# Kernel tuning notes

Measured on AMD Instinct MI355X. Metric: run time of the kernel, lower is better.

## Reference

```python
import jax, jax.numpy as jnp
import numpy as np

DIM, D_STATE, D_CONV, EXPAND = 384, 16, 4, 2
D_INNER = EXPAND * DIM          # 768
DT_RANK = -(-DIM // 16)         # 24
B_, T_, H_, W_ = 2, 8, 16, 16
EPS = 1e-5


def layernorm(x, w, b):
    mu = x.mean(-1, keepdims=True)
    var = ((x - mu) ** 2).mean(-1, keepdims=True)
    return (x - mu) * jax.lax.rsqrt(var + EPS) * w + b


def setup_inputs() -> dict:
    key = jax.random.key(0)
    ks = jax.random.split(key, 12)
    std = 0.02
    x = jax.random.normal(ks[0], (B_, DIM, T_, H_, W_), jnp.float32)
    params = dict(
        ln1_w=jnp.ones((DIM,), jnp.float32),
        ln1_b=jnp.zeros((DIM,), jnp.float32),
        ln2_w=jnp.ones((DIM,), jnp.float32),
        ln2_b=jnp.zeros((DIM,), jnp.float32),
        in_proj_w=std * jax.random.normal(ks[1], (2 * D_INNER, DIM), jnp.float32),
        conv_w=std * jax.random.normal(ks[2], (D_INNER, 1, D_CONV), jnp.float32),
        conv_b=jnp.zeros((D_INNER,), jnp.float32),
        x_proj_w=std * jax.random.normal(ks[3], (DT_RANK + 2 * D_STATE, D_INNER), jnp.float32),
        dt_proj_w=std * jax.random.normal(ks[4], (D_INNER, DT_RANK), jnp.float32),
        dt_proj_b=0.01 * jax.random.normal(ks[5], (D_INNER,), jnp.float32),
        A_log=jnp.log(jnp.broadcast_to(jnp.arange(1, D_STATE + 1, dtype=jnp.float32), (D_INNER, D_STATE))),
        D=jnp.ones((D_INNER,), jnp.float32),
        out_proj_w=std * jax.random.normal(ks[6], (DIM, D_INNER), jnp.float32),
    )
    return {"x": x, **params}


def mamba(xn, in_proj_w, conv_w, conv_b, x_proj_w, dt_proj_w, dt_proj_b, A_log, D, out_proj_w):
    # xn: [B, L, dim]
    B, L, _ = xn.shape
    xz = xn @ in_proj_w.T                      # [B, L, 2*d_inner]
    u, z = jnp.split(xz, 2, axis=-1)
    # causal depthwise conv over tokens
    uc = jnp.transpose(u, (0, 2, 1))           # [B, d_inner, L]
    uc = jax.lax.conv_general_dilated(
        uc, conv_w, window_strides=(1,), padding=[(D_CONV - 1, 0)],
        dimension_numbers=("NCH", "OIH", "NCH"), feature_group_count=D_INNER)
    u = jax.nn.silu(jnp.transpose(uc, (0, 2, 1)) + conv_b)  # [B, L, d_inner]

    dbc = u @ x_proj_w.T                       # [B, L, dt_rank + 2*d_state]
    dt = dbc[..., :DT_RANK]
    Bm = dbc[..., DT_RANK:DT_RANK + D_STATE]   # [B, L, d_state]
    Cm = dbc[..., DT_RANK + D_STATE:]          # [B, L, d_state]
    delta = jax.nn.softplus(dt @ dt_proj_w.T + dt_proj_b)   # [B, L, d_inner]

    A = -jnp.exp(A_log)                        # [d_inner, d_state]
    deltaA = jnp.exp(delta[..., None] * A)                     # [B, L, d_inner, d_state]
    deltaBu = delta[..., None] * Bm[:, :, None, :] * u[..., None]

    def step(h, inp):
        dA, dBu, c = inp                       # [B,d_inner,d_state], [B,d_inner,d_state], [B,d_state]
        h = dA * h + dBu
        y = jnp.einsum("bds,bs->bd", h, c)
        return h, y

    h0 = jnp.zeros((B, D_INNER, D_STATE), xn.dtype)
    xs = (jnp.moveaxis(deltaA, 1, 0), jnp.moveaxis(deltaBu, 1, 0), jnp.moveaxis(Cm, 1, 0))
    _, ys = jax.lax.scan(step, h0, xs)
    y = jnp.moveaxis(ys, 0, 1)                 # [B, L, d_inner]
    y = y + u * D
    y = y * jax.nn.silu(z)
    return y @ out_proj_w.T                    # [B, L, dim]


def reference(x, ln1_w, ln1_b, ln2_w, ln2_b, in_proj_w, conv_w, conv_b,
              x_proj_w, dt_proj_w, dt_proj_b, A_log, D, out_proj_w):
    B, C, T, H, W = x.shape
    L = T * H * W
    x_flat = jnp.transpose(x.reshape(B, C, L), (0, 2, 1))   # [B, L, C]
    x_norm = layernorm(x_flat, ln1_w, ln1_b)
    x_mamba = mamba(x_norm, in_proj_w, conv_w, conv_b, x_proj_w,
                    dt_proj_w, dt_proj_b, A_log, D, out_proj_w)
    x_out = layernorm(x_flat + x_mamba, ln2_w, ln2_b)
    return jnp.transpose(x_out, (0, 2, 1)).reshape(B, C, T, H, W)
```

## Files before the change

kernel.cpp:

```cpp
#include <hip/hip_runtime.h>
#include <hip/hip_bf16.h>

typedef unsigned short u16;
typedef unsigned int   u32;
typedef __attribute__((ext_vector_type(8))) short short8;
typedef __attribute__((ext_vector_type(4))) float f32x4;

#define B_   2
#define L_   2048
#define CDIM 384
#define DI   768
#define DXZ  1536
#define DTR  24
#define DS   16
#define NDBC 56
#define NC2  128
#define TC   16
#define TL   32
#define EPSV 1e-5f

#define OFFW_WIN  0
#define OFFW_WXP  589824
#define OFFW_WOUT 632832
#define TOTW      927744

__device__ __forceinline__ float bf2f(u16 u) {
    union { u32 i; float f; } v; v.i = ((u32)u) << 16; return v.f;
}
__device__ __forceinline__ u16 f2bf(float f) {
    union { float f; u32 i; } v; v.f = f;
    u32 x = v.i;
    u32 r = (x + 0x7FFFu + ((x >> 16) & 1u)) >> 16;
    return (u16)r;
}

__global__ __launch_bounds__(256) void ln1_convert(const float* __restrict__ x,
                                                   const float* __restrict__ w,
                                                   const float* __restrict__ bb,
                                                   u16* __restrict__ xn,
                                                   const float* __restrict__ win,
                                                   const float* __restrict__ wxp,
                                                   const float* __restrict__ wout,
                                                   u16* __restrict__ wdst) {
    __shared__ float tile[CDIM][TL + 1];
    __shared__ float red_s[8][TL];
    __shared__ float red_s2[8][TL];
    __shared__ float mu_s[TL], rs_s[TL];
    int tid = threadIdx.x, blk = blockIdx.x;
    if (blk >= 128) {
        int base = (blk - 128) * 256 + tid;
        for (int e = base; e < TOTW; e += 128 * 256) {
            float v;
            if (e < OFFW_WXP)       v = win[e];
            else if (e < OFFW_WOUT) v = wxp[e - OFFW_WXP];
            else                    v = wout[e - OFFW_WOUT];
            wdst[e] = f2bf(v);
        }
        return;
    }
    int b = blk >> 6;
    int l0 = (blk & 63) * TL;
    int cg = tid >> 5, li = tid & 31;
    const float* xp = x + (size_t)b * CDIM * L_ + l0 + li;
    float s = 0.f, s2 = 0.f;
#pragma unroll
    for (int c = cg; c < CDIM; c += 8) {
        float v = xp[(size_t)c * L_];
        tile[c][li] = v;
        s += v; s2 += v * v;
    }
    red_s[cg][li] = s; red_s2[cg][li] = s2;
    __syncthreads();
    if (tid < TL) {
        float ts = 0.f, ts2 = 0.f;
#pragma unroll
        for (int g = 0; g < 8; g++) { ts += red_s[g][tid]; ts2 += red_s2[g][tid]; }
        float mu = ts / CDIM;
        float var = ts2 / CDIM - mu * mu;
        mu_s[tid] = mu; rs_s[tid] = rsqrtf(var + EPSV);
    }
    __syncthreads();
    int wv = tid >> 6, lane = tid & 63;
#pragma unroll
    for (int r = 0; r < 8; r++) {
        int l = wv * 8 + r;
        float mu = mu_s[l], rs = rs_s[l];
        u16* op = xn + (size_t)(b * L_ + l0 + l) * CDIM;
#pragma unroll
        for (int j = 0; j < 6; j++) {
            int c = lane + 64 * j;
            float t = (tile[c][l] - mu) * rs * w[c] + bb[c];
            op[c] = f2bf(t);
        }
    }
}

template<int KN>
__global__ __launch_bounds__(256) void gemm_in(const u16* __restrict__ A,
                                               const u16* __restrict__ Bm,
                                               u16* __restrict__ Cp, int Nn) {
    int wave = threadIdx.x >> 6, lane = threadIdx.x & 63;
    int wm = wave & 1, wn = wave >> 1;
    int m0 = (blockIdx.x * 2 + wm) * 64;
    int n0 = (blockIdx.y * 2 + wn) * 64;
    int r = lane & 15, q = lane >> 4;
    f32x4 acc[4][4];
#pragma unroll
    for (int i = 0; i < 4; i++)
#pragma unroll
        for (int j = 0; j < 4; j++)
#pragma unroll
            for (int g = 0; g < 4; g++) acc[i][j][g] = 0.f;
#pragma unroll
    for (int k0 = 0; k0 < KN; k0 += 32) {
        short8 af[4], bf[4];
        int ka = k0 + q * 8;
#pragma unroll
        for (int i = 0; i < 4; i++) {
            af[i] = *(const short8*)(A + (size_t)(m0 + i * 16 + r) * KN + ka);
            bf[i] = *(const short8*)(Bm + (size_t)(n0 + i * 16 + r) * KN + ka);
        }
#pragma unroll
        for (int i = 0; i < 4; i++)
#pragma unroll
            for (int j = 0; j < 4; j++)
                acc[i][j] = __builtin_amdgcn_mfma_f32_16x16x32_bf16(af[i], bf[j], acc[i][j], 0, 0, 0);
    }
#pragma unroll
    for (int i = 0; i < 4; i++)
#pragma unroll
        for (int j = 0; j < 4; j++) {
            int col = n0 + j * 16 + r;
#pragma unroll
            for (int g = 0; g < 4; g++)
                Cp[(size_t)(m0 + i * 16 + q * 4 + g) * Nn + col] = f2bf(acc[i][j][g]);
        }
}

__global__ __launch_bounds__(768) void convxp_scan1(const u16* __restrict__ xz,
                                                    const float* __restrict__ cw,
                                                    const float* __restrict__ cb,
                                                    const u16* __restrict__ wxpb,
                                                    const float* __restrict__ alogf,
                                                    const float* __restrict__ wdtf,
                                                    const float* __restrict__ bdtf,
                                                    float* __restrict__ dbc,
                                                    float* __restrict__ chA,
                                                    float* __restrict__ chB) {
    __shared__ __align__(16) u16 uS[TC * DI];
    __shared__ float smR[6][TC][60];
    __shared__ float dbcS[TC][60];
    int tid = threadIdx.x;
    int bc = blockIdx.x;
    int b = bc >> 7, chunk = bc & 127;
    int t0g = b * L_ + chunk * TC;
    float ur[TC];
    {
        int d = tid;
        float4 c4 = ((const float4*)cw)[d];
        float bias = cb[d];
        float w0, w1, w2;
        if (chunk == 0) { w0 = w1 = w2 = 0.f; }
        else {
            w0 = bf2f(xz[(size_t)(t0g - 3) * DXZ + d]);
            w1 = bf2f(xz[(size_t)(t0g - 2) * DXZ + d]);
            w2 = bf2f(xz[(size_t)(t0g - 1) * DXZ + d]);
        }
#pragma unroll
        for (int t = 0; t < TC; t++) {
            float cur = bf2f(xz[(size_t)(t0g + t) * DXZ + d]);
            float acc = bias + w0 * c4.x + w1 * c4.y + w2 * c4.z + cur * c4.w;
            float sg = 1.f / (1.f + __expf(-acc));
            ur[t] = acc * sg;
            uS[t * DI + (d ^ ((t & 7) << 3))] = f2bf(ur[t]);
            w0 = w1; w1 = w2; w2 = cur;
        }
    }
    __syncthreads();
    {
        int wave = tid >> 6, lane = tid & 63;
        int r = lane & 15, q = lane >> 4;
        if (wave < 6) {
            f32x4 acc[4];
#pragma unroll
            for (int j = 0; j < 4; j++)
#pragma unroll
                for (int g = 0; g < 4; g++) acc[j][g] = 0.f;
            short8 zf;
#pragma unroll
            for (int e = 0; e < 8; e++) zf[e] = 0;
            int kb = wave * 128;
#pragma unroll
            for (int k0 = 0; k0 < 128; k0 += 32) {
                int ka = kb + k0 + q * 8;
                short8 af = *(const short8*)(&uS[r * DI + (ka ^ ((r & 7) << 3))]);
                short8 bfv[4];
#pragma unroll
                for (int j = 0; j < 4; j++) {
                    int n = j * 16 + r;
                    bfv[j] = (n < NDBC) ? *(const short8*)(wxpb + (size_t)n * DI + ka) : zf;
                }
#pragma unroll
                for (int j = 0; j < 4; j++)
                    acc[j] = __builtin_amdgcn_mfma_f32_16x16x32_bf16(af, bfv[j], acc[j], 0, 0, 0);
            }
#pragma unroll
            for (int j = 0; j < 4; j++) {
                int col = j * 16 + r;
                if (col < NDBC) {
#pragma unroll
                    for (int g = 0; g < 4; g++)
                        smR[wave][q * 4 + g][col] = acc[j][g];
                }
            }
        }
    }
    __syncthreads();
    for (int e = tid; e < TC * NDBC; e += 768) {
        int row = e / NDBC, col = e - row * NDBC;
        float v = 0.f;
#pragma unroll
        for (int ks = 0; ks < 6; ks++) v += smR[ks][row][col];
        dbcS[row][col] = v;
        dbc[(size_t)(t0g + row) * NDBC + col] = v;
    }
    __syncthreads();
    {
        int d = tid;
        float a[DS], ap[DS], bv[DS], wdtv[DTR];
#pragma unroll
        for (int s = 0; s < DS; s++) { a[s] = -__expf(alogf[d * DS + s]); ap[s] = 1.f; bv[s] = 0.f; }
#pragma unroll
        for (int k = 0; k < DTR; k++) wdtv[k] = wdtf[d * DTR + k];
        float bd = bdtf[d];
#pragma unroll 2
        for (int t = 0; t < TC; t++) {
            float acc = bd;
#pragma unroll
            for (int k = 0; k < DTR; k++) acc += dbcS[t][k] * wdtv[k];
            float dd = (acc > 20.f) ? acc : __logf(1.f + __expf(acc));
            float du = dd * ur[t];
#pragma unroll
            for (int s = 0; s < DS; s++) {
                float dA = __expf(dd * a[s]);
                bv[s] = dA * bv[s] + du * dbcS[t][DTR + s];
                ap[s] *= dA;
            }
        }
        float* pa = chA + (size_t)bc * DS * DI + d;
        float* pb = chB + (size_t)bc * DS * DI + d;
#pragma unroll
        for (int s = 0; s < DS; s++) { pa[(size_t)s * DI] = ap[s]; pb[(size_t)s * DI] = bv[s]; }
    }
}

__global__ __launch_bounds__(256) void scan_mid(const float* __restrict__ chA,
                                                const float* __restrict__ chB,
                                                float* __restrict__ hin) {
    int idx = blockIdx.x * 256 + threadIdx.x;
    int b = idx / (DI * DS);
    int rem = idx - b * (DI * DS);
    float h = 0.f;
#pragma unroll 8
    for (int c = 0; c < NC2; c++) {
        size_t off = ((size_t)(b * NC2 + c) * DI) * DS + rem;
        hin[off] = h;
        h = chA[off] * h + chB[off];
    }
}

__global__ __launch_bounds__(768) void scan2_out_ln2(const u16* __restrict__ xz,
                                                     const float* __restrict__ cw,
                                                     const float* __restrict__ cb,
                                                     const float* __restrict__ dbc,
                                                     const float* __restrict__ alogf,
                                                     const float* __restrict__ wdtf,
                                                     const float* __restrict__ bdtf,
                                                     const float* __restrict__ hin,
                                                     const float* __restrict__ Dwf,
                                                     const u16* __restrict__ woutb,
                                                     const float* __restrict__ x,
                                                     const float* __restrict__ w2,
                                                     const float* __restrict__ b2,
                                                     float* __restrict__ out) {
    __shared__ __align__(16) char uni[TC * 388 * 4];
    __shared__ float smO[TC][388];
    __shared__ float dbcS[TC][60];
    __shared__ float mu_s[TC], rs_s[TC];
    u16* ymS = (u16*)uni;
    float (*xT)[388] = (float(*)[388])uni;
    int tid = threadIdx.x;
    int bc = blockIdx.x;
    int b = bc >> 7, chunk = bc & 127;
    int t0g = b * L_ + chunk * TC;
    for (int e = tid; e < TC * NDBC; e += 768) {
        int row = e / NDBC, col = e - row * NDBC;
        dbcS[row][col] = dbc[(size_t)(t0g + row) * NDBC + col];
    }
    float ur[TC];
    {
        int d = tid;
        float4 c4 = ((const float4*)cw)[d];
        float bias = cb[d];
        float w0, w1, w2c;
        if (chunk == 0) { w0 = w1 = w2c = 0.f; }
        else {
            w0  = bf2f(xz[(size_t)(t0g - 3) * DXZ + d]);
            w1  = bf2f(xz[(size_t)(t0g - 2) * DXZ + d]);
            w2c = bf2f(xz[(size_t)(t0g - 1) * DXZ + d]);
        }
#pragma unroll
        for (int t = 0; t < TC; t++) {
            float cur = bf2f(xz[(size_t)(t0g + t) * DXZ + d]);
            float acc = bias + w0 * c4.x + w1 * c4.y + w2c * c4.z + cur * c4.w;
            float sg = 1.f / (1.f + __expf(-acc));
            ur[t] = acc * sg;
            w0 = w1; w1 = w2c; w2c = cur;
        }
    }
    __syncthreads();
    {
        int d = tid;
        float a[DS], h[DS], wdtv[DTR];
#pragma unroll
        for (int s = 0; s < DS; s++) a[s] = -__expf(alogf[d * DS + s]);
#pragma unroll
        for (int k = 0; k < DTR; k++) wdtv[k] = wdtf[d * DTR + k];
        float bd = bdtf[d];
        const float* hp = hin + (size_t)bc * DS * DI + d;
#pragma unroll
        for (int s = 0; s < DS; s++) h[s] = hp[(size_t)s * DI];
        float dD = Dwf[d];
#pragma unroll 2
        for (int t = 0; t < TC; t++) {
            float acc = bd;
#pragma unroll
            for (int k = 0; k < DTR; k++) acc += dbcS[t][k] * wdtv[k];
            float dd = (acc > 20.f) ? acc : __logf(1.f + __expf(acc));
            float uu = ur[t];
            float du = dd * uu;
            float y = 0.f;
#pragma unroll
            for (int s = 0; s < DS; s++) {
                float dA = __expf(dd * a[s]);
                h[s] = dA * h[s] + du * dbcS[t][DTR + s];
                y += h[s] * dbcS[t][DTR + DS + s];
            }
            float z = bf2f(xz[(size_t)(t0g + t) * DXZ + DI + d]);
            float sg = 1.f / (1.f + __expf(-z));
            ymS[t * DI + (d ^ ((t & 7) << 3))] = f2bf((y + uu * dD) * (z * sg));
        }
    }
    __syncthreads();
    {
        int wave = tid >> 6, lane = tid & 63;
        int r = lane & 15, q = lane >> 4;
        if (wave < 6) {
            int n0 = wave * 64;
            f32x4 acc[4];
#pragma unroll
            for (int j = 0; j < 4; j++)
#pragma unroll
                for (int g = 0; g < 4; g++) acc[j][g] = 0.f;
            int xw = (r & 7) << 3;
#pragma unroll
            for (int k0 = 0; k0 < DI; k0 += 32) {
                int ka = k0 + q * 8;
                short8 af = *(const short8*)(&ymS[r * DI + (ka ^ xw)]);
                short8 bfv[4];
#pragma unroll
                for (int j = 0; j < 4; j++)
                    bfv[j] = *(const short8*)(woutb + (size_t)(n0 + j * 16 + r) * DI + ka);
#pragma unroll
                for (int j = 0; j < 4; j++)
                    acc[j] = __builtin_amdgcn_mfma_f32_16x16x32_bf16(af, bfv[j], acc[j], 0, 0, 0);
            }
#pragma unroll
            for (int j = 0; j < 4; j++) {
                int col = n0 + j * 16 + r;
#pragma unroll
                for (int g = 0; g < 4; g++)
                    smO[q * 4 + g][col] = acc[j][g];
            }
        }
    }
    __syncthreads();
#pragma unroll
    for (int ii = 0; ii < 8; ii++) {
        int e = tid + ii * 768;
        int c = e >> 4, l = e & 15;
        float xv = x[(size_t)b * CDIM * L_ + (size_t)c * L_ + chunk * TC + l];
        float t = xv + smO[l][c];
        xT[l][c] = t;
    }
    __syncthreads();
    {
        int wave = tid >> 6, lane = tid & 63;
        for (int row = wave; row < TC; row += 12) {
            float s = 0.f, s2 = 0.f;
#pragma unroll
            for (int j = 0; j < 6; j++) {
                float t = xT[row][lane + 64 * j];
                s += t; s2 += t * t;
            }
#pragma unroll
            for (int off = 32; off > 0; off >>= 1) { s += __shfl_xor(s, off); s2 += __shfl_xor(s2, off); }
            if (lane == 0) {
                float mu = s / CDIM;
                float var = s2 / CDIM - mu * mu;
                mu_s[row] = mu; rs_s[row] = rsqrtf(var + EPSV);
            }
        }
    }
    __syncthreads();
#pragma unroll
    for (int ii = 0; ii < 8; ii++) {
        int e = tid + ii * 768;
        int c = e >> 4, l = e & 15;
        float t = (xT[l][c] - mu_s[l]) * rs_s[l] * w2[c] + b2[c];
        out[(size_t)b * CDIM * L_ + (size_t)c * L_ + chunk * TC + l] = t;
    }
}

extern "C" void kernel_launch(void* const* d_in, const int* in_sizes, int n_in,
                              void* d_out, int out_size, void* d_ws, size_t ws_size,
                              hipStream_t stream) {
    const float* x    = (const float*)d_in[0];
    const float* ln1w = (const float*)d_in[1];
    const float* ln1b = (const float*)d_in[2];
    const float* ln2w = (const float*)d_in[3];
    const float* ln2b = (const float*)d_in[4];
    const float* win  = (const float*)d_in[5];
    const float* cw   = (const float*)d_in[6];
    const float* cb   = (const float*)d_in[7];
    const float* wxp  = (const float*)d_in[8];
    const float* wdt  = (const float*)d_in[9];
    const float* bdt  = (const float*)d_in[10];
    const float* alog = (const float*)d_in[11];
    const float* Dw   = (const float*)d_in[12];
    const float* wout = (const float*)d_in[13];

    char* ws = (char*)d_ws;
    u16*   wbf    = (u16*)(ws + 0);
    u16*   win_b  = wbf + OFFW_WIN;
    u16*   wxp_b  = wbf + OFFW_WXP;
    u16*   wout_b = wbf + OFFW_WOUT;
    u16*   xn     = (u16*)(ws + 1855488);
    u16*   xz     = (u16*)(ws + 5001216);
    float* dbc    = (float*)(ws + 17584128);
    float* chA    = (float*)(ws + 18501632);
    float* chB    = (float*)(ws + 31084544);
    float* hin    = (float*)(ws + 43667456);

    ln1_convert<<<dim3(256), 256, 0, stream>>>(x, ln1w, ln1b, xn, win, wxp, wout, wbf);
    gemm_in<384><<<dim3(32, 12), 256, 0, stream>>>(xn, win_b, xz, DXZ);
    convxp_scan1<<<dim3(256), 768, 0, stream>>>(xz, cw, cb, wxp_b, alog, wdt, bdt, dbc, chA, chB);
    scan_mid<<<96, 256, 0, stream>>>(chA, chB, hin);
    scan2_out_ln2<<<dim3(256), 768, 0, stream>>>(xz, cw, cb, dbc, alog, wdt, bdt, hin, Dw,
                                                 wout_b, x, ln2w, ln2b, (float*)d_out);
}
```

Measured before the change: 202.5 us.

## Halve scan chunk size to double block count and prefetch state and residual loads

Reduces the chunk length from 16 to 8 tokens, doubling the number of chunks and blocks in the two heavy kernels so that 512 blocks instead of 256 can occupy the GPU's compute units. The MFMA tiles are kept at 16 rows with the unused rows zero-padded, and only the valid half is written back. The scan carry-in state and the residual x values are loaded at kernel start to overlap their latency, and launch bounds add an occupancy hint. In exchange, the sequential mid-scan becomes twice as long, the chunk-state buffers double in size, and half of each MFMA's work is wasted on padding.

```diff
diff --git a/kernel.cpp b/kernel.cpp
--- a/kernel.cpp
+++ b/kernel.cpp
@@ -14,8 +14,8 @@
 #define DTR  24
 #define DS   16
 #define NDBC 56
-#define NC2  128
-#define TC   16
+#define NC2  256
+#define TC   8
 #define TL   32
 #define EPSV 1e-5f
 
@@ -137,22 +137,22 @@
         }
 }
 
-__global__ __launch_bounds__(768) void convxp_scan1(const u16* __restrict__ xz,
-                                                    const float* __restrict__ cw,
-                                                    const float* __restrict__ cb,
-                                                    const u16* __restrict__ wxpb,
-                                                    const float* __restrict__ alogf,
-                                                    const float* __restrict__ wdtf,
-                                                    const float* __restrict__ bdtf,
-                                                    float* __restrict__ dbc,
-                                                    float* __restrict__ chA,
-                                                    float* __restrict__ chB) {
+__global__ __launch_bounds__(768, 6) void convxp_scan1(const u16* __restrict__ xz,
+                                                       const float* __restrict__ cw,
+                                                       const float* __restrict__ cb,
+                                                       const u16* __restrict__ wxpb,
+                                                       const float* __restrict__ alogf,
+                                                       const float* __restrict__ wdtf,
+                                                       const float* __restrict__ bdtf,
+                                                       float* __restrict__ dbc,
+                                                       float* __restrict__ chA,
+                                                       float* __restrict__ chB) {
     __shared__ __align__(16) u16 uS[TC * DI];
     __shared__ float smR[6][TC][60];
     __shared__ float dbcS[TC][60];
     int tid = threadIdx.x;
     int bc = blockIdx.x;
-    int b = bc >> 7, chunk = bc & 127;
+    int b = bc >> 8, chunk = bc & 255;
     int t0g = b * L_ + chunk * TC;
     float ur[TC];
     {
@@ -193,7 +193,7 @@
 #pragma unroll
             for (int k0 = 0; k0 < 128; k0 += 32) {
                 int ka = kb + k0 + q * 8;
-                short8 af = *(const short8*)(&uS[r * DI + (ka ^ ((r & 7) << 3))]);
+                short8 af = (r < TC) ? *(const short8*)(&uS[r * DI + (ka ^ ((r & 7) << 3))]) : zf;
                 short8 bfv[4];
 #pragma unroll
                 for (int j = 0; j < 4; j++) {
@@ -207,7 +207,7 @@
 #pragma unroll
             for (int j = 0; j < 4; j++) {
                 int col = j * 16 + r;
-                if (col < NDBC) {
+                if (col < NDBC && q < 2) {
 #pragma unroll
                     for (int g = 0; g < 4; g++)
                         smR[wave][q * 4 + g][col] = acc[j][g];
@@ -269,20 +269,20 @@
     }
 }
 
-__global__ __launch_bounds__(768) void scan2_out_ln2(const u16* __restrict__ xz,
-                                                     const float* __restrict__ cw,
-                                                     const float* __restrict__ cb,
-                                                     const float* __restrict__ dbc,
-                                                     const float* __restrict__ alogf,
-                                                     const float* __restrict__ wdtf,
-                                                     const float* __restrict__ bdtf,
-                                                     const float* __restrict__ hin,
-                                                     const float* __restrict__ Dwf,
-                                                     const u16* __restrict__ woutb,
-                                                     const float* __restrict__ x,
-                                                     const float* __restrict__ w2,
-                                                     const float* __restrict__ b2,
-                                                     float* __restrict__ out) {
+__global__ __launch_bounds__(768, 6) void scan2_out_ln2(const u16* __restrict__ xz,
+                                                        const float* __restrict__ cw,
+                                                        const float* __restrict__ cb,
+                                                        const float* __restrict__ dbc,
+                                                        const float* __restrict__ alogf,
+                                                        const float* __restrict__ wdtf,
+                                                        const float* __restrict__ bdtf,
+                                                        const float* __restrict__ hin,
+                                                        const float* __restrict__ Dwf,
+                                                        const u16* __restrict__ woutb,
+                                                        const float* __restrict__ x,
+                                                        const float* __restrict__ w2,
+                                                        const float* __restrict__ b2,
+                                                        float* __restrict__ out) {
     __shared__ __align__(16) char uni[TC * 388 * 4];
     __shared__ float smO[TC][388];
     __shared__ float dbcS[TC][60];
@@ -291,8 +291,22 @@
     float (*xT)[388] = (float(*)[388])uni;
     int tid = threadIdx.x;
     int bc = blockIdx.x;
-    int b = bc >> 7, chunk = bc & 127;
+    int b = bc >> 8, chunk = bc & 255;
     int t0g = b * L_ + chunk * TC;
+
+    float h[DS];
+    {
+        const float* hp = hin + (size_t)bc * DS * DI + tid;
+#pragma unroll
+        for (int s = 0; s < DS; s++) h[s] = hp[(size_t)s * DI];
+    }
+    float xr[4];
+#pragma unroll
+    for (int ii = 0; ii < 4; ii++) {
+        int e = tid + ii * 768;
+        int c = e >> 3, l = e & 7;
+        xr[ii] = x[(size_t)b * CDIM * L_ + (size_t)c * L_ + chunk * TC + l];
+    }
     for (int e = tid; e < TC * NDBC; e += 768) {
         int row = e / NDBC, col = e - row * NDBC;
         dbcS[row][col] = dbc[(size_t)(t0g + row) * NDBC + col];
@@ -321,15 +335,12 @@
     __syncthreads();
     {
         int d = tid;
-        float a[DS], h[DS], wdtv[DTR];
+        float a[DS], wdtv[DTR];
 #pragma unroll
         for (int s = 0; s < DS; s++) a[s] = -__expf(alogf[d * DS + s]);
 #pragma unroll
         for (int k = 0; k < DTR; k++) wdtv[k] = wdtf[d * DTR + k];
         float bd = bdtf[d];
-        const float* hp = hin + (size_t)bc * DS * DI + d;
-#pragma unroll
-        for (int s = 0; s < DS; s++) h[s] = hp[(size_t)s * DI];
         float dD = Dwf[d];
 #pragma unroll 2
         for (int t = 0; t < TC; t++) {
@@ -362,11 +373,14 @@
             for (int j = 0; j < 4; j++)
 #pragma unroll
                 for (int g = 0; g < 4; g++) acc[j][g] = 0.f;
+            short8 zf;
+#pragma unroll
+            for (int e = 0; e < 8; e++) zf[e] = 0;
             int xw = (r & 7) << 3;
 #pragma unroll
             for (int k0 = 0; k0 < DI; k0 += 32) {
                 int ka = k0 + q * 8;
-                short8 af = *(const short8*)(&ymS[r * DI + (ka ^ xw)]);
+                short8 af = (r < TC) ? *(const short8*)(&ymS[r * DI + (ka ^ xw)]) : zf;
                 short8 bfv[4];
 #pragma unroll
                 for (int j = 0; j < 4; j++)
@@ -375,28 +389,29 @@
                 for (int j = 0; j < 4; j++)
                     acc[j] = __builtin_amdgcn_mfma_f32_16x16x32_bf16(af, bfv[j], acc[j], 0, 0, 0);
             }
-#pragma unroll
-            for (int j = 0; j < 4; j++) {
-                int col = n0 + j * 16 + r;
-#pragma unroll
-                for (int g = 0; g < 4; g++)
-                    smO[q * 4 + g][col] = acc[j][g];
-            }
-        }
-    }
-    __syncthreads();
-#pragma unroll
-    for (int ii = 0; ii < 8; ii++) {
+            if (q < 2) {
+#pragma unroll
+                for (int j = 0; j < 4; j++) {
+                    int col = n0 + j * 16 + r;
+#pragma unroll
+                    for (int g = 0; g < 4; g++)
+                        smO[q * 4 + g][col] = acc[j][g];
+                }
+            }
+        }
+    }
+    __syncthreads();
+#pragma unroll
+    for (int ii = 0; ii < 4; ii++) {
         int e = tid + ii * 768;
-        int c = e >> 4, l = e & 15;
-        float xv = x[(size_t)b * CDIM * L_ + (size_t)c * L_ + chunk * TC + l];
-        float t = xv + smO[l][c];
-        xT[l][c] = t;
+        int c = e >> 3, l = e & 7;
+        xT[l][c] = xr[ii] + smO[l][c];
     }
     __syncthreads();
     {
         int wave = tid >> 6, lane = tid & 63;
-        for (int row = wave; row < TC; row += 12) {
+        if (wave < TC) {
+            int row = wave;
             float s = 0.f, s2 = 0.f;
 #pragma unroll
             for (int j = 0; j < 6; j++) {
@@ -414,9 +429,9 @@
     }
     __syncthreads();
 #pragma unroll
-    for (int ii = 0; ii < 8; ii++) {
+    for (int ii = 0; ii < 4; ii++) {
         int e = tid + ii * 768;
-        int c = e >> 4, l = e & 15;
+        int c = e >> 3, l = e & 7;
         float t = (xT[l][c] - mu_s[l]) * rs_s[l] * w2[c] + b2[c];
         out[(size_t)b * CDIM * L_ + (size_t)c * L_ + chunk * TC + l] = t;
     }
@@ -449,13 +464,13 @@
     u16*   xz     = (u16*)(ws + 5001216);
     float* dbc    = (float*)(ws + 17584128);
     float* chA    = (float*)(ws + 18501632);
-    float* chB    = (float*)(ws + 31084544);
-    float* hin    = (float*)(ws + 43667456);
+    float* chB    = (float*)(ws + 43667456);
+    float* hin    = (float*)(ws + 68833280);
 
     ln1_convert<<<dim3(256), 256, 0, stream>>>(x, ln1w, ln1b, xn, win, wxp, wout, wbf);
     gemm_in<384><<<dim3(32, 12), 256, 0, stream>>>(xn, win_b, xz, DXZ);
-    convxp_scan1<<<dim3(256), 768, 0, stream>>>(xz, cw, cb, wxp_b, alog, wdt, bdt, dbc, chA, chB);
+    convxp_scan1<<<dim3(512), 768, 0, stream>>>(xz, cw, cb, wxp_b, alog, wdt, bdt, dbc, chA, chB);
     scan_mid<<<96, 256, 0, stream>>>(chA, chB, hin);
-    scan2_out_ln2<<<dim3(256), 768, 0, stream>>>(xz, cw, cb, dbc, alog, wdt, bdt, hin, Dw,
+    scan2_out_ln2<<<dim3(512), 768, 0, stream>>>(xz, cw, cb, dbc, alog, wdt, bdt, hin, Dw,
                                                  wout_b, x, ln2w, ln2b, (float*)d_out);
 }
```

After: 342.8 us. 1.69x slower.

## Fuse LayerNorm1 into in-projection GEMM with on-the-fly bf16 staging in LDS

Applied to the files above, without the earlier changes.

Merges the LayerNorm1 kernel and the input-projection GEMM into one kernel. Each 128x128 tile block computes row statistics from x, normalizes and converts A tiles to bf16 in LDS, and converts the fp32 in_proj weights to bf16 while staging them. Only three extra blocks remain to convert the x_proj and out_proj weights. This drops one launch and the xn round-trip through global memory, but x is re-read and renormalized by each of the 12 N-tile blocks, and the k-loop now has two barriers per step with no double buffering.

```diff
diff --git a/kernel.cpp b/kernel.cpp
--- a/kernel.cpp
+++ b/kernel.cpp
@@ -34,75 +34,50 @@
     return (u16)r;
 }
 
-__global__ __launch_bounds__(256) void ln1_convert(const float* __restrict__ x,
-                                                   const float* __restrict__ w,
-                                                   const float* __restrict__ bb,
-                                                   u16* __restrict__ xn,
+__global__ __launch_bounds__(256) void ln1_gemm_in(const float* __restrict__ x,
+                                                   const float* __restrict__ w1,
+                                                   const float* __restrict__ b1,
                                                    const float* __restrict__ win,
                                                    const float* __restrict__ wxp,
                                                    const float* __restrict__ wout,
-                                                   u16* __restrict__ wdst) {
-    __shared__ float tile[CDIM][TL + 1];
-    __shared__ float red_s[8][TL];
-    __shared__ float red_s2[8][TL];
-    __shared__ float mu_s[TL], rs_s[TL];
+                                                   u16* __restrict__ wdst,
+                                                   u16* __restrict__ xz) {
+    __shared__ __align__(16) u16 As[128 * 40];
+    __shared__ __align__(16) u16 Bs[128 * 40];
+    __shared__ float mu_s[128], rs_s[128];
     int tid = threadIdx.x, blk = blockIdx.x;
-    if (blk >= 128) {
-        int base = (blk - 128) * 256 + tid;
-        for (int e = base; e < TOTW; e += 128 * 256) {
-            float v;
-            if (e < OFFW_WXP)       v = win[e];
-            else if (e < OFFW_WOUT) v = wxp[e - OFFW_WXP];
-            else                    v = wout[e - OFFW_WOUT];
-            wdst[e] = f2bf(v);
+    if (blk >= 384) {
+        int base = (blk - 384) * 256 + tid;
+        for (int e = base; e < TOTW - OFFW_WXP; e += 3 * 256) {
+            float v = (e < OFFW_WOUT - OFFW_WXP) ? wxp[e]
+                                                 : wout[e - (OFFW_WOUT - OFFW_WXP)];
+            wdst[OFFW_WXP + e] = f2bf(v);
         }
         return;
     }
-    int b = blk >> 6;
-    int l0 = (blk & 63) * TL;
-    int cg = tid >> 5, li = tid & 31;
-    const float* xp = x + (size_t)b * CDIM * L_ + l0 + li;
-    float s = 0.f, s2 = 0.f;
-#pragma unroll
-    for (int c = cg; c < CDIM; c += 8) {
-        float v = xp[(size_t)c * L_];
-        tile[c][li] = v;
-        s += v; s2 += v * v;
-    }
-    red_s[cg][li] = s; red_s2[cg][li] = s2;
-    __syncthreads();
-    if (tid < TL) {
-        float ts = 0.f, ts2 = 0.f;
-#pragma unroll
-        for (int g = 0; g < 8; g++) { ts += red_s[g][tid]; ts2 += red_s2[g][tid]; }
-        float mu = ts / CDIM;
-        float var = ts2 / CDIM - mu * mu;
-        mu_s[tid] = mu; rs_s[tid] = rsqrtf(var + EPSV);
-    }
-    __syncthreads();
-    int wv = tid >> 6, lane = tid & 63;
-#pragma unroll
-    for (int r = 0; r < 8; r++) {
-        int l = wv * 8 + r;
-        float mu = mu_s[l], rs = rs_s[l];
-        u16* op = xn + (size_t)(b * L_ + l0 + l) * CDIM;
-#pragma unroll
-        for (int j = 0; j < 6; j++) {
-            int c = lane + 64 * j;
-            float t = (tile[c][l] - mu) * rs * w[c] + bb[c];
-            op[c] = f2bf(t);
-        }
-    }
-}
-
-template<int KN>
-__global__ __launch_bounds__(256) void gemm_in(const u16* __restrict__ A,
-                                               const u16* __restrict__ Bm,
-                                               u16* __restrict__ Cp, int Nn) {
-    int wave = threadIdx.x >> 6, lane = threadIdx.x & 63;
+    int mt = blk & 31, nt = blk >> 5;
+    int m0 = mt * 128;
+    int b = m0 >> 11;
+    int l0 = m0 & 2047;
+    int n0 = nt * 128;
+    {
+        int r = tid >> 1, hf = tid & 1;
+        const float* xp = x + (size_t)b * CDIM * L_ + l0 + r;
+        float s = 0.f, s2 = 0.f;
+        for (int c = hf * 192; c < hf * 192 + 192; c++) {
+            float v = xp[(size_t)c * L_];
+            s += v; s2 += v * v;
+        }
+        s += __shfl_xor(s, 1); s2 += __shfl_xor(s2, 1);
+        if (hf == 0) {
+            float mu = s / CDIM;
+            float var = s2 / CDIM - mu * mu;
+            mu_s[r] = mu; rs_s[r] = rsqrtf(var + EPSV);
+        }
+    }
+    __syncthreads();
+    int lane = tid & 63, wave = tid >> 6;
     int wm = wave & 1, wn = wave >> 1;
-    int m0 = (blockIdx.x * 2 + wm) * 64;
-    int n0 = (blockIdx.y * 2 + wn) * 64;
     int r = lane & 15, q = lane >> 4;
     f32x4 acc[4][4];
 #pragma unroll
@@ -111,29 +86,48 @@
         for (int j = 0; j < 4; j++)
 #pragma unroll
             for (int g = 0; g < 4; g++) acc[i][j][g] = 0.f;
-#pragma unroll
-    for (int k0 = 0; k0 < KN; k0 += 32) {
+    u32* As32 = (u32*)As;
+    u32* Bs32 = (u32*)Bs;
+    for (int k0 = 0; k0 < CDIM; k0 += 32) {
+#pragma unroll
+        for (int rep = 0; rep < 8; rep++) {
+            int e = rep * 256 + tid;
+            int row = e & 127, kp = e >> 7;
+            int c = k0 + kp * 2;
+            const float* xp = x + (size_t)b * CDIM * L_ + l0 + row;
+            float v0 = (xp[(size_t)c * L_]       - mu_s[row]) * rs_s[row] * w1[c]     + b1[c];
+            float v1 = (xp[(size_t)(c + 1) * L_] - mu_s[row]) * rs_s[row] * w1[c + 1] + b1[c + 1];
+            As32[row * 20 + kp] = (u32)f2bf(v0) | ((u32)f2bf(v1) << 16);
+        }
+#pragma unroll
+        for (int rep = 0; rep < 8; rep++) {
+            int e = rep * 256 + tid;
+            int kp = e & 15, row = e >> 4;
+            const float* wp = win + (size_t)(n0 + row) * CDIM + k0 + kp * 2;
+            Bs32[row * 20 + kp] = (u32)f2bf(wp[0]) | ((u32)f2bf(wp[1]) << 16);
+        }
+        __syncthreads();
         short8 af[4], bf[4];
-        int ka = k0 + q * 8;
 #pragma unroll
         for (int i = 0; i < 4; i++) {
-            af[i] = *(const short8*)(A + (size_t)(m0 + i * 16 + r) * KN + ka);
-            bf[i] = *(const short8*)(Bm + (size_t)(n0 + i * 16 + r) * KN + ka);
+            af[i] = *(const short8*)(&As[(wm * 64 + i * 16 + r) * 40 + q * 8]);
+            bf[i] = *(const short8*)(&Bs[(wn * 64 + i * 16 + r) * 40 + q * 8]);
         }
 #pragma unroll
         for (int i = 0; i < 4; i++)
 #pragma unroll
             for (int j = 0; j < 4; j++)
                 acc[i][j] = __builtin_amdgcn_mfma_f32_16x16x32_bf16(af[i], bf[j], acc[i][j], 0, 0, 0);
+        __syncthreads();
     }
 #pragma unroll
     for (int i = 0; i < 4; i++)
 #pragma unroll
         for (int j = 0; j < 4; j++) {
-            int col = n0 + j * 16 + r;
+            int col = n0 + wn * 64 + j * 16 + r;
 #pragma unroll
             for (int g = 0; g < 4; g++)
-                Cp[(size_t)(m0 + i * 16 + q * 4 + g) * Nn + col] = f2bf(acc[i][j][g]);
+                xz[(size_t)(m0 + wm * 64 + i * 16 + q * 4 + g) * DXZ + col] = f2bf(acc[i][j][g]);
         }
 }
 
@@ -390,8 +384,7 @@
         int e = tid + ii * 768;
         int c = e >> 4, l = e & 15;
         float xv = x[(size_t)b * CDIM * L_ + (size_t)c * L_ + chunk * TC + l];
-        float t = xv + smO[l][c];
-        xT[l][c] = t;
+        xT[l][c] = xv + smO[l][c];
     }
     __syncthreads();
     {
@@ -442,18 +435,15 @@
 
     char* ws = (char*)d_ws;
     u16*   wbf    = (u16*)(ws + 0);
-    u16*   win_b  = wbf + OFFW_WIN;
     u16*   wxp_b  = wbf + OFFW_WXP;
     u16*   wout_b = wbf + OFFW_WOUT;
-    u16*   xn     = (u16*)(ws + 1855488);
     u16*   xz     = (u16*)(ws + 5001216);
     float* dbc    = (float*)(ws + 17584128);
     float* chA    = (float*)(ws + 18501632);
     float* chB    = (float*)(ws + 31084544);
     float* hin    = (float*)(ws + 43667456);
 
-    ln1_convert<<<dim3(256), 256, 0, stream>>>(x, ln1w, ln1b, xn, win, wxp, wout, wbf);
-    gemm_in<384><<<dim3(32, 12), 256, 0, stream>>>(xn, win_b, xz, DXZ);
+    ln1_gemm_in<<<dim3(387), 256, 0, stream>>>(x, ln1w, ln1b, win, wxp, wout, wbf, xz);
     convxp_scan1<<<dim3(256), 768, 0, stream>>>(xz, cw, cb, wxp_b, alog, wdt, bdt, dbc, chA, chB);
     scan_mid<<<96, 256, 0, stream>>>(chA, chB, hin);
     scan2_out_ln2<<<dim3(256), 768, 0, stream>>>(xz, cw, cb, dbc, alog, wdt, bdt, hin, Dw,
```

Result: slower. 242.6 us (+19.8%).
